# Performance work log

Hardware: AMD Instinct MI355X
Metric: run time of the kernel (lower is better)

Reference implementation:

```python
import jax, jax.numpy as jnp
import numpy as np

B = 1024          # graphs (games)
NPG = 12          # nodes per hand (to_dense_batch max_num_nodes=12)
N = B * NPG       # nodes per node type
EPG = 72          # edges per graph per edge type
E = B * EPG
CARD = 32         # card embedding dim
HID = 256         # hidden_dim
H = 4             # attention heads
L = 3             # num_layers
FIN = 128         # final_dim
LRELU_SLOPE = float(FIN)  # faithful to nn.LeakyReLU(final_dim) bug


def _make_edges(key):
    k1, k2 = jax.random.split(key)
    g = jnp.repeat(jnp.arange(B, dtype=jnp.int32), EPG)
    src = g * NPG + jax.random.randint(k1, (E,), 0, NPG, dtype=jnp.int32)
    dst = g * NPG + jax.random.randint(k2, (E,), 0, NPG, dtype=jnp.int32)
    return jnp.stack([src, dst])


def setup_inputs() -> dict:
    key = jax.random.key(0)
    ks = jax.random.split(key, 24)
    def nrm(k, shape, fan):
        return jax.random.normal(k, shape, jnp.float32) / np.float32(np.sqrt(fan))
    inp = {
        'x_my': jax.random.normal(ks[0], (N, CARD), jnp.float32),
        'x_opp': jax.random.normal(ks[1], (N, CARD), jnp.float32),
        'edge_beats': _make_edges(ks[2]),
        'edge_loses': _make_edges(ks[3]),
        'edge_rev_beats': _make_edges(ks[4]),
        'edge_rev_loses': _make_edges(ks[5]),
        'batch_my': jnp.repeat(jnp.arange(B, dtype=jnp.int32), NPG),
        # input encoder
        'enc_W': nrm(ks[6], (CARD, HID), CARD), 'enc_b': jnp.zeros((HID,), jnp.float32),
        # GATv2 params, axis1 indexes {0: beats(my->opp), 1: rev_loses_to(opp->my)}
        'gat_Wl': nrm(ks[7], (L, 2, HID, H * HID), HID),
        'gat_bl': jnp.zeros((L, 2, H * HID), jnp.float32),
        'gat_Wr': nrm(ks[8], (L, 2, HID, H * HID), HID),
        'gat_br': jnp.zeros((L, 2, H * HID), jnp.float32),
        'gat_att': nrm(ks[9], (L, 2, H, HID), HID),
        'gat_bias': jnp.zeros((L, 2, HID), jnp.float32),
        # CGConv params, axis1 indexes {0: loses_to(my->opp), 1: rev_beats(opp->my)}
        'cg_Wf': nrm(ks[10], (L, 2, 2 * HID, HID), 2 * HID),
        'cg_bf': jnp.zeros((L, 2, HID), jnp.float32),
        'cg_Ws': nrm(ks[11], (L, 2, 2 * HID, HID), 2 * HID),
        'cg_bs': jnp.zeros((L, 2, HID), jnp.float32),
        # nodewise linear per layer
        'node_W': nrm(ks[12], (L, HID, HID), HID),
        'node_b': jnp.zeros((L, HID), jnp.float32),
        # final encoder
        'fin_W1': nrm(ks[13], (HID, FIN), HID), 'fin_b1': jnp.zeros((FIN,), jnp.float32),
        'fin_W2': nrm(ks[14], (FIN, 1), FIN), 'fin_b2': jnp.zeros((1,), jnp.float32),
    }
    return inp


def _gatv2(x_src, x_dst, edge, Wl, bl, Wr, br, att, bias):
    # PyG GATv2Conv, concat=False, add_self_loops=False, negative_slope=0.2
    Nd = x_dst.shape[0]
    xl = (x_src @ Wl + bl).reshape(-1, H, HID)   # [Ns,H,C]
    xr = (x_dst @ Wr + br).reshape(-1, H, HID)   # [Nd,H,C]
    src, dst = edge[0], edge[1]
    e = jax.nn.leaky_relu(xl[src] + xr[dst], 0.2)            # [E,H,C]
    alpha = jnp.einsum('ehc,hc->eh', e, att)                 # [E,H]
    m = jax.ops.segment_max(alpha, dst, num_segments=Nd)     # softmax by dst
    a = jnp.exp(alpha - m[dst])
    denom = jax.ops.segment_sum(a, dst, num_segments=Nd)
    a = a / (denom[dst] + 1e-16)
    out = jax.ops.segment_sum(a[:, :, None] * xl[src], dst, num_segments=Nd)
    return out.mean(axis=1) + bias                           # mean over heads


def _cgconv(x_src, x_dst, edge, Wf, bf, Ws, bs):
    # PyG CGConv: z = [x_i(dst), x_j(src)]; sigmoid gate * softplus; sum; residual
    src, dst = edge[0], edge[1]
    z = jnp.concatenate([x_dst[dst], x_src[src]], axis=-1)   # [E,2*HID]
    msg = jax.nn.sigmoid(z @ Wf + bf) * jax.nn.softplus(z @ Ws + bs)
    return x_dst + jax.ops.segment_sum(msg, dst, num_segments=x_dst.shape[0])


def reference(x_my, x_opp, edge_beats, edge_loses, edge_rev_beats, edge_rev_loses,
              batch_my, enc_W, enc_b, gat_Wl, gat_bl, gat_Wr, gat_br, gat_att,
              gat_bias, cg_Wf, cg_bf, cg_Ws, cg_bs, node_W, node_b,
              fin_W1, fin_b1, fin_W2, fin_b2):
    h_my = x_my @ enc_W + enc_b
    h_opp = x_opp @ enc_W + enc_b
    for l in range(L):
        # destination opponent_hand: GAT(beats) + CG(loses_to)  (HeteroConv aggr='sum')
        opp_new = _gatv2(h_my, h_opp, edge_beats, gat_Wl[l, 0], gat_bl[l, 0],
                         gat_Wr[l, 0], gat_br[l, 0], gat_att[l, 0], gat_bias[l, 0]) \
                + _cgconv(h_my, h_opp, edge_loses, cg_Wf[l, 0], cg_bf[l, 0],
                          cg_Ws[l, 0], cg_bs[l, 0])
        # destination my_hand: CG(rev_beats) + GAT(rev_loses_to)
        my_new = _cgconv(h_opp, h_my, edge_rev_beats, cg_Wf[l, 1], cg_bf[l, 1],
                         cg_Ws[l, 1], cg_bs[l, 1]) \
               + _gatv2(h_opp, h_my, edge_rev_loses, gat_Wl[l, 1], gat_bl[l, 1],
                        gat_Wr[l, 1], gat_br[l, 1], gat_att[l, 1], gat_bias[l, 1])
        h_my = my_new @ node_W[l] + node_b[l]
        h_opp = opp_new @ node_W[l] + node_b[l]
    f = jax.nn.leaky_relu(h_my @ fin_W1 + fin_b1, LRELU_SLOPE)
    logits = f @ fin_W2 + fin_b2                              # [N,1]
    # to_dense_batch with exactly NPG sorted nodes per graph == reshape
    return logits.reshape(B, NPG)
```

## Files before the change

kernel.cpp:

```cpp
#include <hip/hip_runtime.h>

#define NNODES 12288
#define ETOT   73728
#define NGR    1024
#define LOG2E  1.442695041f
#define LN2    0.6931471806f

typedef __attribute__((ext_vector_type(8))) short short8;
typedef __attribute__((ext_vector_type(4))) float f32x4;

__device__ __forceinline__ unsigned short f2b(float f) {
  return __builtin_bit_cast(unsigned short, (__bf16)f);
}
__device__ __forceinline__ float b2f(unsigned short u) {
  return __uint_as_float(((unsigned)u) << 16);
}
__device__ __forceinline__ void load_lds16(const void* g, void* l) {
  __builtin_amdgcn_global_load_lds(
      (const __attribute__((address_space(1))) unsigned int*)g,
      (__attribute__((address_space(3))) unsigned int*)l, 16, 0, 0);
}
__device__ __forceinline__ unsigned fenc(float f) {
  unsigned u = __float_as_uint(f);
  return (u & 0x80000000u) ? ~u : (u | 0x80000000u);
}
__device__ __forceinline__ float fdec(unsigned e) {
  unsigned u = (e & 0x80000000u) ? (e & 0x7FFFFFFFu) : ~e;
  return __uint_as_float(u);
}

__device__ __forceinline__ const unsigned short* pnode(
    const unsigned short* P, int col0, int node) {
  return P + ((size_t)(col0 >> 7) * NNODES + node) * 128 + (col0 & 127);
}

__global__ void pack_kernel(
    const float* __restrict__ gat_Wl, const float* __restrict__ gat_Wr,
    const float* __restrict__ cg_Wf, const float* __restrict__ cg_Ws,
    const float* __restrict__ node_W, const float* __restrict__ enc_W,
    const float* __restrict__ fin_W1,
    const float* __restrict__ gat_bl, const float* __restrict__ gat_br,
    const float* __restrict__ cg_bf, const float* __restrict__ cg_bs,
    const float* __restrict__ x_my, const float* __restrict__ x_opp,
    unsigned short* __restrict__ wt_my, unsigned short* __restrict__ wt_opp,
    unsigned short* __restrict__ node_wt, unsigned short* __restrict__ enc_wt,
    unsigned short* __restrict__ fin_w1t,
    float* __restrict__ bias_my, float* __restrict__ bias_opp,
    unsigned short* __restrict__ xb)
{
  int idx = blockIdx.x * 256 + threadIdx.x;
  if (idx < 2 * 2359296) {
    int which = idx >= 2359296;
    int t = which ? idx - 2359296 : idx;
    int l = t / 786432;
    int r = t - l * 786432;
    int j = r & 7, lane = (r >> 3) & 63, blk = r >> 9;
    int kb = blk & 7, nb = blk >> 3;
    int n = nb * 16 + (lane & 15);
    int k = kb * 32 + (lane >> 4) * 8 + j;
    float v;
    if (!which) {
      if (n < 1024)      v = gat_Wl[((l*2+0)*256 + k)*1024 + n];
      else if (n < 2048) v = gat_Wr[((l*2+1)*256 + k)*1024 + (n-1024)];
      else if (n < 2304) v = cg_Wf[((l*2+0)*512 + 256 + k)*256 + (n-2048)];
      else if (n < 2560) v = cg_Ws[((l*2+0)*512 + 256 + k)*256 + (n-2304)];
      else if (n < 2816) v = cg_Wf[((l*2+1)*512 + k)*256 + (n-2560)];
      else               v = cg_Ws[((l*2+1)*512 + k)*256 + (n-2816)];
      wt_my[t] = f2b(v);
    } else {
      if (n < 1024)      v = gat_Wr[((l*2+0)*256 + k)*1024 + n];
      else if (n < 2048) v = gat_Wl[((l*2+1)*256 + k)*1024 + (n-1024)];
      else if (n < 2304) v = cg_Wf[((l*2+0)*512 + k)*256 + (n-2048)];
      else if (n < 2560) v = cg_Ws[((l*2+0)*512 + k)*256 + (n-2304)];
      else if (n < 2816) v = cg_Wf[((l*2+1)*512 + 256 + k)*256 + (n-2560)];
      else               v = cg_Ws[((l*2+1)*512 + 256 + k)*256 + (n-2816)];
      wt_opp[t] = f2b(v);
    }
    return;
  }
  idx -= 2 * 2359296;
  if (idx < 196608) {
    int l = idx / 65536, r = idx - l * 65536;
    int j = r & 7, lane = (r >> 3) & 63, blk = r >> 9;
    int kb = blk & 7, nb = blk >> 3;
    int n = nb * 16 + (lane & 15);
    int k = kb * 32 + (lane >> 4) * 8 + j;
    node_wt[idx] = f2b(node_W[(l*256 + k)*256 + n]);
    return;
  }
  idx -= 196608;
  if (idx < 8192) {
    int r = idx;
    int j = r & 7, lane = (r >> 3) & 63, blk = r >> 9;
    int nb = blk;
    int n = nb * 16 + (lane & 15);
    int k = (lane >> 4) * 8 + j;
    enc_wt[idx] = f2b(enc_W[k*256 + n]);
    return;
  }
  idx -= 8192;
  if (idx < 32768) {
    int r = idx;
    int j = r & 7, lane = (r >> 3) & 63, blk = r >> 9;
    int kb = blk & 7, nb = blk >> 3;
    int n = nb * 16 + (lane & 15);
    int k = kb * 32 + (lane >> 4) * 8 + j;
    fin_w1t[idx] = f2b(fin_W1[k*128 + n]);
    return;
  }
  idx -= 32768;
  if (idx < 9216) {
    int l = idx / 3072, n = idx - l * 3072;
    float v;
    if (n < 1024)      v = gat_bl[(l*2+0)*1024 + n];
    else if (n < 2048) v = gat_br[(l*2+1)*1024 + (n-1024)];
    else if (n < 2560) v = 0.f;
    else if (n < 2816) v = cg_bf[(l*2+1)*256 + (n-2560)];
    else               v = cg_bs[(l*2+1)*256 + (n-2816)];
    bias_my[idx] = v;
    return;
  }
  idx -= 9216;
  if (idx < 9216) {
    int l = idx / 3072, n = idx - l * 3072;
    float v;
    if (n < 1024)      v = gat_br[(l*2+0)*1024 + n];
    else if (n < 2048) v = gat_bl[(l*2+1)*1024 + (n-1024)];
    else if (n < 2304) v = cg_bf[(l*2+0)*256 + (n-2048)];
    else if (n < 2560) v = cg_bs[(l*2+0)*256 + (n-2304)];
    else               v = 0.f;
    bias_opp[idx] = v;
    return;
  }
  idx -= 9216;
  if (idx < 2 * 393216) {
    xb[idx] = f2b(idx < 393216 ? x_my[idx] : x_opp[idx - 393216]);
  }
}

__global__ __launch_bounds__(256) void gemm64(
    const unsigned short* __restrict__ A, const unsigned short* __restrict__ Ab,
    int lda,
    const unsigned short* __restrict__ Wp, const unsigned short* __restrict__ Wpb,
    const float* __restrict__ bias, const float* __restrict__ biasb,
    unsigned short* __restrict__ C, unsigned short* __restrict__ Cb,
    int ldc, int K, int act, int bx_split)
{
  __shared__ __align__(16) unsigned short lA[64 * 256];
  const int tid = threadIdx.x;
  const int lane = tid & 63;
  const int w = tid >> 6;
  const int wr = w >> 1, wc = w & 1;
  const int r0 = lane & 15, kq = lane >> 4;
  const int KT = K >> 5;
  const int gm = (K >> 3) - 1;
  const int rmask = gm > 7 ? 7 : gm;
  const int gsh = __popc((unsigned)gm);

  const unsigned short *Ap, *Wsel;
  const float* bp;
  unsigned short* Cp;
  int tileM;
  if ((int)blockIdx.x < bx_split) {
    Ap = A;  Wsel = Wp;  bp = bias;  Cp = C;  tileM = blockIdx.x * 64;
  } else {
    Ap = Ab; Wsel = Wpb; bp = biasb; Cp = Cb; tileM = (blockIdx.x - bx_split) * 64;
  }
  const int tileN = blockIdx.y * 128;

  for (int rd = 0; rd < KT; ++rd) {
    int idx = rd * 256 + tid;
    int row = idx >> gsh;
    int g = idx & gm;
    load_lds16(Ap + (size_t)(tileM + row) * lda + ((g ^ (row & rmask)) << 3),
               (char*)lA + idx * 16);
  }

  const int nblk0 = (tileN >> 4) + wc * 4;
  const unsigned short* wn0 = Wsel + ((size_t)(nblk0 + 0) * KT * 64 + lane) * 8;
  const unsigned short* wn1 = Wsel + ((size_t)(nblk0 + 1) * KT * 64 + lane) * 8;
  const unsigned short* wn2 = Wsel + ((size_t)(nblk0 + 2) * KT * 64 + lane) * 8;
  const unsigned short* wn3 = Wsel + ((size_t)(nblk0 + 3) * KT * 64 + lane) * 8;

  short8 b0_0 = *(const short8*)wn0;
  short8 b0_1 = *(const short8*)wn1;
  short8 b0_2 = *(const short8*)wn2;
  short8 b0_3 = *(const short8*)wn3;
  short8 b1_0 = b0_0, b1_1 = b0_1, b1_2 = b0_2, b1_3 = b0_3;
  if (KT > 1) {
    b1_0 = *(const short8*)(wn0 + 512);
    b1_1 = *(const short8*)(wn1 + 512);
    b1_2 = *(const short8*)(wn2 + 512);
    b1_3 = *(const short8*)(wn3 + 512);
  }

  f32x4 acc[2][4];
#pragma unroll
  for (int m = 0; m < 2; ++m)
#pragma unroll
    for (int n = 0; n < 4; ++n)
      acc[m][n] = (f32x4){0.f, 0.f, 0.f, 0.f};

  const int rb0 = (wr * 32 + r0) * K;
  const int rb1 = (wr * 32 + 16 + r0) * K;
  const int rx = r0 & rmask;

  __syncthreads();

  for (int kt = 0; kt < KT; ++kt) {
    short8 b2_0 = b1_0, b2_1 = b1_1, b2_2 = b1_2, b2_3 = b1_3;
    if (kt + 2 < KT) {
      const int o = (kt + 2) * 512;
      b2_0 = *(const short8*)(wn0 + o);
      b2_1 = *(const short8*)(wn1 + o);
      b2_2 = *(const short8*)(wn2 + o);
      b2_3 = *(const short8*)(wn3 + o);
    }
    const int p = (((kt << 2) + kq) ^ rx) * 8;
    short8 af0 = *(const short8*)&lA[rb0 + p];
    short8 af1 = *(const short8*)&lA[rb1 + p];
    acc[0][0] = __builtin_amdgcn_mfma_f32_16x16x32_bf16(b0_0, af0, acc[0][0], 0, 0, 0);
    acc[0][1] = __builtin_amdgcn_mfma_f32_16x16x32_bf16(b0_1, af0, acc[0][1], 0, 0, 0);
    acc[0][2] = __builtin_amdgcn_mfma_f32_16x16x32_bf16(b0_2, af0, acc[0][2], 0, 0, 0);
    acc[0][3] = __builtin_amdgcn_mfma_f32_16x16x32_bf16(b0_3, af0, acc[0][3], 0, 0, 0);
    acc[1][0] = __builtin_amdgcn_mfma_f32_16x16x32_bf16(b0_0, af1, acc[1][0], 0, 0, 0);
    acc[1][1] = __builtin_amdgcn_mfma_f32_16x16x32_bf16(b0_1, af1, acc[1][1], 0, 0, 0);
    acc[1][2] = __builtin_amdgcn_mfma_f32_16x16x32_bf16(b0_2, af1, acc[1][2], 0, 0, 0);
    acc[1][3] = __builtin_amdgcn_mfma_f32_16x16x32_bf16(b0_3, af1, acc[1][3], 0, 0, 0);
    b0_0 = b1_0; b0_1 = b1_1; b0_2 = b1_2; b0_3 = b1_3;
    b1_0 = b2_0; b1_1 = b2_1; b1_2 = b2_2; b1_3 = b2_3;
  }

  unsigned short* cT = lA;
  __syncthreads();
#pragma unroll
  for (int m = 0; m < 2; ++m) {
    const int rl = wr * 32 + m * 16 + r0;
#pragma unroll
    for (int n = 0; n < 4; ++n) {
      const int cl = wc * 64 + n * 16 + kq * 4;
      const f32x4 bv = *(const f32x4*)&bp[tileN + cl];
      float v0 = acc[m][n][0] + bv[0];
      float v1 = acc[m][n][1] + bv[1];
      float v2 = acc[m][n][2] + bv[2];
      float v3 = acc[m][n][3] + bv[3];
      if (act) {
        v0 = v0 > 0.f ? v0 : 128.f * v0;
        v1 = v1 > 0.f ? v1 : 128.f * v1;
        v2 = v2 > 0.f ? v2 : 128.f * v2;
        v3 = v3 > 0.f ? v3 : 128.f * v3;
      }
      uint2 pk;
      pk.x = (unsigned)f2b(v0) | ((unsigned)f2b(v1) << 16);
      pk.y = (unsigned)f2b(v2) | ((unsigned)f2b(v3) << 16);
      *(uint2*)&cT[rl * 132 + cl] = pk;
    }
  }
  __syncthreads();
#pragma unroll
  for (int it = 0; it < 4; ++it) {
    const int idx = it * 256 + tid;
    const int row = idx >> 4, ch = idx & 15;
    const uint4 val = *(const uint4*)&cT[row * 132 + ch * 8];
    *(uint4*)(Cp + (size_t)(tileM + row) * ldc + tileN + ch * 8) = val;
  }
}

__global__ __launch_bounds__(256) void gemm64p(
    const unsigned short* __restrict__ A, const unsigned short* __restrict__ Ab,
    const unsigned short* __restrict__ Wp, const unsigned short* __restrict__ Wpb,
    const float* __restrict__ bias, const float* __restrict__ biasb,
    unsigned short* __restrict__ C, unsigned short* __restrict__ Cb,
    int bx_split)
{
  const int K = 256, KT = 8;
  __shared__ __align__(16) unsigned short lA[64 * 256];
  __shared__ __align__(16) unsigned short cT[64 * 132];
  const int tid = threadIdx.x;
  const int lane = tid & 63;
  const int w = tid >> 6;
  const int wr = w >> 1, wc = w & 1;
  const int r0 = lane & 15, kq = lane >> 4;

  const unsigned short *Ap, *Wsel;
  const float* bp;
  unsigned short* Cp;
  int tileM;
  if ((int)blockIdx.x < bx_split) {
    Ap = A;  Wsel = Wp;  bp = bias;  Cp = C;  tileM = blockIdx.x * 64;
  } else {
    Ap = Ab; Wsel = Wpb; bp = biasb; Cp = Cb; tileM = (blockIdx.x - bx_split) * 64;
  }

  for (int rd = 0; rd < KT; ++rd) {
    int idx = rd * 256 + tid;
    int row = idx >> 5;
    int g = idx & 31;
    load_lds16(Ap + (size_t)(tileM + row) * K + ((g ^ (row & 7)) << 3),
               (char*)lA + idx * 16);
  }

  const int rb0 = (wr * 32 + r0) * K;
  const int rb1 = (wr * 32 + 16 + r0) * K;
  const int rx = r0 & 7;

  __syncthreads();

  for (int nn = 0; nn < 12; ++nn) {
    const int cb = (int)blockIdx.y * 12 + nn;
    const int tileN = cb * 128;
    const int nblk0 = (tileN >> 4) + wc * 4;
    const unsigned short* wn0 = Wsel + ((size_t)(nblk0 + 0) * KT * 64 + lane) * 8;
    const unsigned short* wn1 = Wsel + ((size_t)(nblk0 + 1) * KT * 64 + lane) * 8;
    const unsigned short* wn2 = Wsel + ((size_t)(nblk0 + 2) * KT * 64 + lane) * 8;
    const unsigned short* wn3 = Wsel + ((size_t)(nblk0 + 3) * KT * 64 + lane) * 8;

    short8 b0_0 = *(const short8*)wn0;
    short8 b0_1 = *(const short8*)wn1;
    short8 b0_2 = *(const short8*)wn2;
    short8 b0_3 = *(const short8*)wn3;
    short8 b1_0 = *(const short8*)(wn0 + 512);
    short8 b1_1 = *(const short8*)(wn1 + 512);
    short8 b1_2 = *(const short8*)(wn2 + 512);
    short8 b1_3 = *(const short8*)(wn3 + 512);

    f32x4 acc[2][4];
#pragma unroll
    for (int m = 0; m < 2; ++m)
#pragma unroll
      for (int n = 0; n < 4; ++n)
        acc[m][n] = (f32x4){0.f, 0.f, 0.f, 0.f};

    for (int kt = 0; kt < KT; ++kt) {
      short8 b2_0 = b1_0, b2_1 = b1_1, b2_2 = b1_2, b2_3 = b1_3;
      if (kt + 2 < KT) {
        const int o = (kt + 2) * 512;
        b2_0 = *(const short8*)(wn0 + o);
        b2_1 = *(const short8*)(wn1 + o);
        b2_2 = *(const short8*)(wn2 + o);
        b2_3 = *(const short8*)(wn3 + o);
      }
      const int p = (((kt << 2) + kq) ^ rx) * 8;
      short8 af0 = *(const short8*)&lA[rb0 + p];
      short8 af1 = *(const short8*)&lA[rb1 + p];
      acc[0][0] = __builtin_amdgcn_mfma_f32_16x16x32_bf16(b0_0, af0, acc[0][0], 0, 0, 0);
      acc[0][1] = __builtin_amdgcn_mfma_f32_16x16x32_bf16(b0_1, af0, acc[0][1], 0, 0, 0);
      acc[0][2] = __builtin_amdgcn_mfma_f32_16x16x32_bf16(b0_2, af0, acc[0][2], 0, 0, 0);
      acc[0][3] = __builtin_amdgcn_mfma_f32_16x16x32_bf16(b0_3, af0, acc[0][3], 0, 0, 0);
      acc[1][0] = __builtin_amdgcn_mfma_f32_16x16x32_bf16(b0_0, af1, acc[1][0], 0, 0, 0);
      acc[1][1] = __builtin_amdgcn_mfma_f32_16x16x32_bf16(b0_1, af1, acc[1][1], 0, 0, 0);
      acc[1][2] = __builtin_amdgcn_mfma_f32_16x16x32_bf16(b0_2, af1, acc[1][2], 0, 0, 0);
      acc[1][3] = __builtin_amdgcn_mfma_f32_16x16x32_bf16(b0_3, af1, acc[1][3], 0, 0, 0);
      b0_0 = b1_0; b0_1 = b1_1; b0_2 = b1_2; b0_3 = b1_3;
      b1_0 = b2_0; b1_1 = b2_1; b1_2 = b2_2; b1_3 = b2_3;
    }

    __syncthreads();
#pragma unroll
    for (int m = 0; m < 2; ++m) {
      const int rl = wr * 32 + m * 16 + r0;
#pragma unroll
      for (int n = 0; n < 4; ++n) {
        const int cl = wc * 64 + n * 16 + kq * 4;
        const f32x4 bv = *(const f32x4*)&bp[tileN + cl];
        uint2 pk;
        pk.x = (unsigned)f2b(acc[m][n][0] + bv[0]) |
               ((unsigned)f2b(acc[m][n][1] + bv[1]) << 16);
        pk.y = (unsigned)f2b(acc[m][n][2] + bv[2]) |
               ((unsigned)f2b(acc[m][n][3] + bv[3]) << 16);
        *(uint2*)&cT[rl * 132 + cl] = pk;
      }
    }
    __syncthreads();
    unsigned short* dstb = Cp + ((size_t)cb * NNODES + tileM) * 128;
#pragma unroll
    for (int it = 0; it < 4; ++it) {
      const int idx = it * 256 + tid;
      const uint4 val = *(const uint4*)&cT[(idx >> 4) * 132 + (idx & 15) * 8];
      *(uint4*)(dstb + (size_t)idx * 8) = val;
    }
  }
}

#define SX 260
__global__ __launch_bounds__(256) void gat_edge(
    const unsigned short* __restrict__ proj_my,
    const unsigned short* __restrict__ proj_op,
    const int* __restrict__ e_beats, const int* __restrict__ e_rl,
    const float* __restrict__ attL, const float* __restrict__ gbiasL,
    unsigned short* __restrict__ gat_op, unsigned short* __restrict__ gat_my)
{
  __shared__ __align__(16) unsigned short xl[48 * SX];
  __shared__ __align__(16) float attS[4 * SX];
  __shared__ float alphaU[288];
  __shared__ float wU[288];
  __shared__ unsigned mU[48];
  __shared__ float denS[48];
  __shared__ __align__(16) float A2f[12 * 48];
  __shared__ int pmap[144], multI[144], uniqP[144], nuniqS;
  __shared__ unsigned char se8[72], de8[72];
  const int bid = blockIdx.x, tid = threadIdx.x;
  const int dir = bid >= NGR;
  const int g = dir ? bid - NGR : bid;
  const int base = g * 12;

  const unsigned short *Psrc, *Pdst;
  int pcol0;
  const int* edges;
  const float* att;
  const float* gbias;
  unsigned short* outp;
  if (!dir) {
    Psrc = proj_my; Pdst = proj_op; pcol0 = 0;
    edges = e_beats; att = attL; gbias = gbiasL; outp = gat_op;
  } else {
    Psrc = proj_op; Pdst = proj_my; pcol0 = 1024;
    edges = e_rl; att = attL + 1024; gbias = gbiasL + 256; outp = gat_my;
  }

  if (tid < 72) {
    se8[tid] = (unsigned char)(edges[g * 72 + tid] - base);
    de8[tid] = (unsigned char)(edges[ETOT + g * 72 + tid] - base);
  }
  if (tid < 144) { pmap[tid] = -1; multI[tid] = 0; }
  if (tid == 0) nuniqS = 0;
  if (tid < 48) { mU[tid] = 0u; denS[tid] = 0.f; }
  for (int i = tid; i < 576; i += 256) A2f[i] = 0.f;
  for (int i = tid; i < 1024; i += 256)
    attS[(i >> 8) * SX + (i & 255)] = att[i];
  for (int i = tid; i < 3072; i += 256) {
    int s = i >> 8, c4 = (i & 255) * 4;
    int h = c4 >> 8, cc = c4 & 255;
    *(ushort4*)&xl[(h * 12 + s) * SX + cc] =
        *(const ushort4*)pnode(Psrc, pcol0 + c4, base + s);
  }
  __syncthreads();

  if (tid < 72) {
    const int p = (int)de8[tid] * 12 + (int)se8[tid];
    atomicAdd(&multI[p], 1);
    if (atomicCAS(&pmap[p], -1, 0) == -1) {
      const int u = atomicAdd(&nuniqS, 1);
      uniqP[u] = p;
    }
  }
  __syncthreads();
  const int NU4 = nuniqS * 4;

  for (int t = tid; t < NU4; t += 256) {
    const int u = t >> 2, h = t & 3;
    const int p = uniqP[u];
    const int d = p / 12, s = p - d * 12;
    const unsigned short* prA = pnode(Pdst, pcol0 + h * 256, base + d);
    float sum = 0.f;
#pragma unroll
    for (int half = 0; half < 2; ++half) {
      const unsigned short* pr = prA + (size_t)half * (NNODES * 128);
      const unsigned short* pl = &xl[(h * 12 + s) * SX + half * 128];
      const f32x4* pa = (const f32x4*)&attS[h * SX + half * 128];
      for (int q = 0; q < 32; ++q) {
        ushort4 a4 = *(const ushort4*)(pl + q * 4);
        ushort4 b4 = *(const ushort4*)(pr + q * 4);
        f32x4 av = pa[q];
        float v0 = b2f(a4.x) + b2f(b4.x); v0 = fmaxf(v0, 0.2f * v0);
        float v1 = b2f(a4.y) + b2f(b4.y); v1 = fmaxf(v1, 0.2f * v1);
        float v2 = b2f(a4.z) + b2f(b4.z); v2 = fmaxf(v2, 0.2f * v2);
        float v3 = b2f(a4.w) + b2f(b4.w); v3 = fmaxf(v3, 0.2f * v3);
        sum = fmaf(v0, av.x, sum); sum = fmaf(v1, av.y, sum);
        sum = fmaf(v2, av.z, sum); sum = fmaf(v3, av.w, sum);
      }
    }
    sum *= LOG2E;
    alphaU[t] = sum;
    atomicMax(&mU[d * 4 + h], fenc(sum));
  }
  __syncthreads();

  for (int t = tid; t < NU4; t += 256) {
    const int u = t >> 2, h = t & 3;
    const int p = uniqP[u];
    const int d = p / 12;
    const float m = fdec(mU[d * 4 + h]);
    const float wv = __builtin_amdgcn_exp2f(alphaU[t] - m);
    wU[t] = wv;
    atomicAdd(&denS[d * 4 + h], (float)multI[p] * wv);
  }
  __syncthreads();

  for (int t = tid; t < NU4; t += 256) {
    const int u = t >> 2, h = t & 3;
    const int p = uniqP[u];
    const int d = p / 12, s = p - d * 12;
    const float inv = 0.25f * __builtin_amdgcn_rcpf(denS[d * 4 + h] + 1e-16f);
    A2f[d * 48 + h * 12 + s] = (float)multI[p] * wU[t] * inv;
  }
  __syncthreads();

  {
    const int c = tid;
    float xlv[48];
#pragma unroll
    for (int j = 0; j < 48; ++j) xlv[j] = b2f(xl[j * SX + c]);
    const float gb = gbias[c];
#pragma unroll
    for (int d = 0; d < 12; ++d) {
      const f32x4* arow = (const f32x4*)&A2f[d * 48];
      float s = 0.f;
#pragma unroll
      for (int jj = 0; jj < 12; ++jj) {
        f32x4 a4 = arow[jj];
        s = fmaf(a4.x, xlv[jj * 4 + 0], s);
        s = fmaf(a4.y, xlv[jj * 4 + 1], s);
        s = fmaf(a4.z, xlv[jj * 4 + 2], s);
        s = fmaf(a4.w, xlv[jj * 4 + 3], s);
      }
      outp[(size_t)(base + d) * 256 + c] = f2b(s + gb);
    }
  }
}

__global__ __launch_bounds__(256) void cg_fused(
    const unsigned short* __restrict__ proj_my,
    const unsigned short* __restrict__ proj_op,
    unsigned short* __restrict__ Hmy, unsigned short* __restrict__ Hopp,
    const unsigned short* __restrict__ gat_my, const unsigned short* __restrict__ gat_op,
    const int* __restrict__ e_loses, const int* __restrict__ e_rb,
    const unsigned short* __restrict__ node_wtL, const float* __restrict__ node_bL)
{
  __shared__ __align__(8) unsigned short df[3072], dsb[3072];
  __shared__ __align__(8) unsigned short sfb[3072], ssb[3072];
  __shared__ __align__(16) unsigned short At[16 * 264];
  __shared__ unsigned char srcl[12 * 80];
  __shared__ int cnt[12];
  __shared__ int se_[72], de_[72];
  const int bid = blockIdx.x, tid = threadIdx.x;
  const int dir = bid >= NGR;
  const int g = dir ? bid - NGR : bid;
  const int base = g * 12;

  const unsigned short *Pd, *Ps, *gatp;
  unsigned short *Hout;
  int fcol, scol;
  const int* edges;
  if (!dir) {
    Pd = proj_op; Ps = proj_my; fcol = 2048; scol = 2304;
    Hout = Hopp; gatp = gat_op; edges = e_loses;
  } else {
    Pd = proj_my; Ps = proj_op; fcol = 2560; scol = 2816;
    Hout = Hmy; gatp = gat_my; edges = e_rb;
  }

  if (tid < 72) {
    se_[tid] = edges[g * 72 + tid] - base;
    de_[tid] = edges[ETOT + g * 72 + tid] - base;
  }
  for (int i = tid; i < 768; i += 256) {
    int s = i >> 6, c4 = (i & 63) * 4;
    const int node = base + s;
    *(ushort4*)&df[s * 256 + c4]  = *(const ushort4*)pnode(Pd, fcol + c4, node);
    *(ushort4*)&dsb[s * 256 + c4] = *(const ushort4*)pnode(Pd, scol + c4, node);
    *(ushort4*)&sfb[s * 256 + c4] = *(const ushort4*)pnode(Ps, fcol + c4, node);
    *(ushort4*)&ssb[s * 256 + c4] = *(const ushort4*)pnode(Ps, scol + c4, node);
  }
  const int c = tid;
  float hv[12], gv[12];
#pragma unroll
  for (int d = 0; d < 12; ++d) {
    const size_t o = (size_t)(base + d) * 256 + c;
    hv[d] = b2f(Hout[o]);
    gv[d] = b2f(gatp[o]);
  }
  __syncthreads();
  if (tid < 12) {
    int n = 0;
    for (int e = 0; e < 72; ++e)
      if (de_[e] == tid) srcl[tid * 80 + (n++)] = (unsigned char)se_[e];
    cnt[tid] = n;
  }
  __syncthreads();
  for (int d = 0; d < 12; ++d) {
    const float fd = b2f(df[d * 256 + c]);
    const float sd = b2f(dsb[d * 256 + c]);
    const int n = cnt[d];
    float acc = 0.f;
    for (int j = 0; j < n; ++j) {
      const int s = srcl[d * 80 + j];
      const float zf = fd + b2f(sfb[s * 256 + c]);
      const float zs = sd + b2f(ssb[s * 256 + c]);
      const float gate = __builtin_amdgcn_rcpf(1.f + __builtin_amdgcn_exp2f(-LOG2E * zf));
      const float e2 = __builtin_amdgcn_exp2f(-LOG2E * fabsf(zs));
      const float sp = fmaxf(zs, 0.f) + LN2 * __builtin_amdgcn_logf(1.f + e2);
      acc = fmaf(gate, sp, acc);
    }
    At[d * 264 + c] = f2b(hv[d] + gv[d] + acc);
  }
  __syncthreads();
  {
    const int w = tid >> 6, lane = tid & 63;
    const int r0 = lane & 15, kq = lane >> 4;
#pragma unroll
    for (int n = 0; n < 4; ++n) {
      const unsigned short* wb = node_wtL + ((size_t)(w * 4 + n) * 8) * 512 + lane * 8;
      f32x4 a = (f32x4){0.f, 0.f, 0.f, 0.f};
#pragma unroll
      for (int kt = 0; kt < 8; ++kt) {
        short8 wf = *(const short8*)(wb + kt * 512);
        short8 af = *(const short8*)&At[r0 * 264 + kt * 32 + kq * 8];
        a = __builtin_amdgcn_mfma_f32_16x16x32_bf16(wf, af, a, 0, 0, 0);
      }
      if (r0 < 12) {
        const int col0 = w * 64 + n * 16 + kq * 4;
        const f32x4 bv = *(const f32x4*)&node_bL[col0];
        uint2 pk;
        pk.x = (unsigned)f2b(a[0] + bv[0]) | ((unsigned)f2b(a[1] + bv[1]) << 16);
        pk.y = (unsigned)f2b(a[2] + bv[2]) | ((unsigned)f2b(a[3] + bv[3]) << 16);
        *(uint2*)(Hout + (size_t)(base + r0) * 256 + col0) = pk;
      }
    }
  }
}

__global__ __launch_bounds__(256) void logits_kernel(
    const unsigned short* __restrict__ f, const float* __restrict__ W2,
    const float* __restrict__ b2, float* __restrict__ out)
{
  const int node = blockIdx.x * 4 + (threadIdx.x >> 6);
  const int lane = threadIdx.x & 63;
  const size_t o = (size_t)node * 128 + lane * 2;
  float s = b2f(f[o]) * W2[lane * 2] + b2f(f[o + 1]) * W2[lane * 2 + 1];
  for (int d = 32; d > 0; d >>= 1) s += __shfl_down(s, d, 64);
  if (lane == 0) out[node] = s + b2[0];
}

extern "C" void kernel_launch(void* const* d_in, const int* in_sizes, int n_in,
                              void* d_out, int out_size, void* d_ws, size_t ws_size,
                              hipStream_t stream) {
  const float* x_my    = (const float*)d_in[0];
  const float* x_opp   = (const float*)d_in[1];
  const int*   e_beats = (const int*)d_in[2];
  const int*   e_loses = (const int*)d_in[3];
  const int*   e_rb    = (const int*)d_in[4];
  const int*   e_rl    = (const int*)d_in[5];
  const float* enc_W   = (const float*)d_in[7];
  const float* enc_b   = (const float*)d_in[8];
  const float* gat_Wl  = (const float*)d_in[9];
  const float* gat_bl  = (const float*)d_in[10];
  const float* gat_Wr  = (const float*)d_in[11];
  const float* gat_br  = (const float*)d_in[12];
  const float* gat_att = (const float*)d_in[13];
  const float* gat_bsp = (const float*)d_in[14];
  const float* cg_Wf   = (const float*)d_in[15];
  const float* cg_bf   = (const float*)d_in[16];
  const float* cg_Ws   = (const float*)d_in[17];
  const float* cg_bs   = (const float*)d_in[18];
  const float* node_W  = (const float*)d_in[19];
  const float* node_b  = (const float*)d_in[20];
  const float* fin_W1  = (const float*)d_in[21];
  const float* fin_b1  = (const float*)d_in[22];
  const float* fin_W2  = (const float*)d_in[23];
  const float* fin_b2  = (const float*)d_in[24];

  char* wsp = (char*)d_ws;
  size_t off = 0;
  auto alloc = [&](size_t b) { char* p = wsp + off; off += (b + 255) & ~(size_t)255; return p; };
  unsigned short* wt_my   = (unsigned short*)alloc((size_t)2359296 * 2);
  unsigned short* wt_opp  = (unsigned short*)alloc((size_t)2359296 * 2);
  unsigned short* node_wt = (unsigned short*)alloc((size_t)196608 * 2);
  unsigned short* enc_wt  = (unsigned short*)alloc((size_t)8192 * 2);
  unsigned short* fin_w1t = (unsigned short*)alloc((size_t)32768 * 2);
  float*          bias_my = (float*)alloc((size_t)9216 * 4);
  float*          bias_op = (float*)alloc((size_t)9216 * 4);
  unsigned short* xb      = (unsigned short*)alloc((size_t)786432 * 2);
  unsigned short* Hb      = (unsigned short*)alloc((size_t)2 * NNODES * 256 * 2);
  unsigned short* proj_my = (unsigned short*)alloc((size_t)NNODES * 3072 * 2);
  unsigned short* proj_op = (unsigned short*)alloc((size_t)NNODES * 3072 * 2);
  unsigned short* gat_my  = (unsigned short*)alloc((size_t)NNODES * 256 * 2);
  unsigned short* gat_op  = (unsigned short*)alloc((size_t)NNODES * 256 * 2);
  unsigned short* fbuf    = (unsigned short*)alloc((size_t)NNODES * 128 * 2);

  const int PACK_TOTAL = 2 * 2359296 + 196608 + 8192 + 32768 + 2 * 9216 + 2 * 393216;
  pack_kernel<<<(PACK_TOTAL + 255) / 256, 256, 0, stream>>>(
      gat_Wl, gat_Wr, cg_Wf, cg_Ws, node_W, enc_W, fin_W1,
      gat_bl, gat_br, cg_bf, cg_bs, x_my, x_opp,
      wt_my, wt_opp, node_wt, enc_wt, fin_w1t, bias_my, bias_op, xb);

  unsigned short* Hmy  = Hb;
  unsigned short* Hopp = Hb + (size_t)NNODES * 256;

  gemm64<<<dim3(384, 2), 256, 0, stream>>>(
      xb, xb, 32, enc_wt, enc_wt, enc_b, enc_b, Hb, Hb, 256, 32, 0, 384);

  for (int l = 0; l < 3; ++l) {
    gemm64p<<<dim3(384, 2), 256, 0, stream>>>(
        Hmy, Hopp,
        wt_my + (size_t)l * 786432, wt_opp + (size_t)l * 786432,
        bias_my + l * 3072, bias_op + l * 3072,
        proj_my, proj_op, 192);
    gat_edge<<<2 * NGR, 256, 0, stream>>>(
        proj_my, proj_op, e_beats, e_rl,
        gat_att + l * 2048, gat_bsp + l * 512, gat_op, gat_my);
    cg_fused<<<2 * NGR, 256, 0, stream>>>(
        proj_my, proj_op, Hmy, Hopp, gat_my, gat_op,
        e_loses, e_rb,
        node_wt + (size_t)l * 65536, node_b + l * 256);
  }

  gemm64<<<dim3(192, 1), 256, 0, stream>>>(
      Hmy, Hmy, 256, fin_w1t, fin_w1t, fin_b1, fin_b1, fbuf, fbuf, 128, 256, 1, 192);
  logits_kernel<<<NNODES / 4, 256, 0, stream>>>(fbuf, fin_W2, fin_b2, (float*)d_out);
}
```

Baseline: 516.2 us.

## Compute GAT attention scores with 16-lane groups per destination-head and shuffle softmax

Replaces the per-unique-edge serial 256-channel dot products and shared-memory atomic max/sum passes with a layout where each 16-lane group owns one (destination, head) pair. Each lane handles 16 channels, reduces with cross-lane shuffles, and then does the softmax max and denominator in registers. This removes several barriers, the float-encoded atomics and the long serial loop per thread, and spreads the global reads of destination projections across lanes. The cost is redundant work for destinations with few sources. The code also assumes at most 16 distinct sources per destination, which holds because a hand has 12 nodes.

```diff
diff --git a/kernel.cpp b/kernel.cpp
--- a/kernel.cpp
+++ b/kernel.cpp
@@ -19,14 +19,6 @@
   __builtin_amdgcn_global_load_lds(
       (const __attribute__((address_space(1))) unsigned int*)g,
       (__attribute__((address_space(3))) unsigned int*)l, 16, 0, 0);
-}
-__device__ __forceinline__ unsigned fenc(float f) {
-  unsigned u = __float_as_uint(f);
-  return (u & 0x80000000u) ? ~u : (u | 0x80000000u);
-}
-__device__ __forceinline__ float fdec(unsigned e) {
-  unsigned u = (e & 0x80000000u) ? (e & 0x7FFFFFFFu) : ~e;
-  return __uint_as_float(u);
 }
 
 __device__ __forceinline__ const unsigned short* pnode(
@@ -392,13 +384,11 @@
 {
   __shared__ __align__(16) unsigned short xl[48 * SX];
   __shared__ __align__(16) float attS[4 * SX];
-  __shared__ float alphaU[288];
-  __shared__ float wU[288];
-  __shared__ unsigned mU[48];
-  __shared__ float denS[48];
   __shared__ __align__(16) float A2f[12 * 48];
-  __shared__ int pmap[144], multI[144], uniqP[144], nuniqS;
-  __shared__ unsigned char se8[72], de8[72];
+  __shared__ int multI[144];
+  __shared__ unsigned char srcG[12][12];
+  __shared__ unsigned char multG[12][12];
+  __shared__ int cntG[12];
   const int bid = blockIdx.x, tid = threadIdx.x;
   const int dir = bid >= NGR;
   const int g = dir ? bid - NGR : bid;
@@ -418,14 +408,14 @@
     edges = e_rl; att = attL + 1024; gbias = gbiasL + 256; outp = gat_my;
   }
 
+  if (tid < 144) multI[tid] = 0;
+  for (int i = tid; i < 576; i += 256) A2f[i] = 0.f;
+  __syncthreads();
   if (tid < 72) {
-    se8[tid] = (unsigned char)(edges[g * 72 + tid] - base);
-    de8[tid] = (unsigned char)(edges[ETOT + g * 72 + tid] - base);
-  }
-  if (tid < 144) { pmap[tid] = -1; multI[tid] = 0; }
-  if (tid == 0) nuniqS = 0;
-  if (tid < 48) { mU[tid] = 0u; denS[tid] = 0.f; }
-  for (int i = tid; i < 576; i += 256) A2f[i] = 0.f;
+    const int s = edges[g * 72 + tid] - base;
+    const int d = edges[ETOT + g * 72 + tid] - base;
+    atomicAdd(&multI[d * 12 + s], 1);
+  }
   for (int i = tid; i < 1024; i += 256)
     attS[(i >> 8) * SX + (i & 255)] = att[i];
   for (int i = tid; i < 3072; i += 256) {
@@ -436,63 +426,88 @@
   }
   __syncthreads();
 
-  if (tid < 72) {
-    const int p = (int)de8[tid] * 12 + (int)se8[tid];
-    atomicAdd(&multI[p], 1);
-    if (atomicCAS(&pmap[p], -1, 0) == -1) {
-      const int u = atomicAdd(&nuniqS, 1);
-      uniqP[u] = p;
-    }
-  }
-  __syncthreads();
-  const int NU4 = nuniqS * 4;
-
-  for (int t = tid; t < NU4; t += 256) {
-    const int u = t >> 2, h = t & 3;
-    const int p = uniqP[u];
-    const int d = p / 12, s = p - d * 12;
-    const unsigned short* prA = pnode(Pdst, pcol0 + h * 256, base + d);
-    float sum = 0.f;
-#pragma unroll
-    for (int half = 0; half < 2; ++half) {
-      const unsigned short* pr = prA + (size_t)half * (NNODES * 128);
-      const unsigned short* pl = &xl[(h * 12 + s) * SX + half * 128];
-      const f32x4* pa = (const f32x4*)&attS[h * SX + half * 128];
-      for (int q = 0; q < 32; ++q) {
-        ushort4 a4 = *(const ushort4*)(pl + q * 4);
-        ushort4 b4 = *(const ushort4*)(pr + q * 4);
-        f32x4 av = pa[q];
-        float v0 = b2f(a4.x) + b2f(b4.x); v0 = fmaxf(v0, 0.2f * v0);
-        float v1 = b2f(a4.y) + b2f(b4.y); v1 = fmaxf(v1, 0.2f * v1);
-        float v2 = b2f(a4.z) + b2f(b4.z); v2 = fmaxf(v2, 0.2f * v2);
-        float v3 = b2f(a4.w) + b2f(b4.w); v3 = fmaxf(v3, 0.2f * v3);
-        sum = fmaf(v0, av.x, sum); sum = fmaf(v1, av.y, sum);
-        sum = fmaf(v2, av.z, sum); sum = fmaf(v3, av.w, sum);
-      }
-    }
-    sum *= LOG2E;
-    alphaU[t] = sum;
-    atomicMax(&mU[d * 4 + h], fenc(sum));
-  }
-  __syncthreads();
-
-  for (int t = tid; t < NU4; t += 256) {
-    const int u = t >> 2, h = t & 3;
-    const int p = uniqP[u];
-    const int d = p / 12;
-    const float m = fdec(mU[d * 4 + h]);
-    const float wv = __builtin_amdgcn_exp2f(alphaU[t] - m);
-    wU[t] = wv;
-    atomicAdd(&denS[d * 4 + h], (float)multI[p] * wv);
-  }
-  __syncthreads();
-
-  for (int t = tid; t < NU4; t += 256) {
-    const int u = t >> 2, h = t & 3;
-    const int p = uniqP[u];
-    const int d = p / 12, s = p - d * 12;
-    const float inv = 0.25f * __builtin_amdgcn_rcpf(denS[d * 4 + h] + 1e-16f);
-    A2f[d * 48 + h * 12 + s] = (float)multI[p] * wU[t] * inv;
+  if (tid < 12) {
+    int n = 0;
+    for (int s = 0; s < 12; ++s) {
+      const int m = multI[tid * 12 + s];
+      if (m > 0) { srcG[tid][n] = (unsigned char)s; multG[tid][n] = (unsigned char)m; ++n; }
+    }
+    cntG[tid] = n;
+  }
+  __syncthreads();
+
+  for (int r = 0; r < 3; ++r) {
+    const int slot = r * 256 + tid;
+    const int g16 = slot >> 4, lane16 = slot & 15;
+    const int d = g16 >> 2, h = g16 & 3;
+    const int cnt = cntG[d];
+    const int ch0 = lane16 * 16;
+    const unsigned short* prp = pnode(Pdst, pcol0 + h * 256 + ch0, base + d);
+    const ushort4 xr0 = *(const ushort4*)(prp);
+    const ushort4 xr1 = *(const ushort4*)(prp + 4);
+    const ushort4 xr2 = *(const ushort4*)(prp + 8);
+    const ushort4 xr3 = *(const ushort4*)(prp + 12);
+    const float* pa = &attS[h * SX + ch0];
+    const f32x4 at0 = *(const f32x4*)(pa);
+    const f32x4 at1 = *(const f32x4*)(pa + 4);
+    const f32x4 at2 = *(const f32x4*)(pa + 8);
+    const f32x4 at3 = *(const f32x4*)(pa + 12);
+
+    float myalpha = -1e30f;
+    for (int j = 0; j < cnt; ++j) {
+      const int s = srcG[d][j];
+      const unsigned short* pl = &xl[(h * 12 + s) * SX + ch0];
+      float p = 0.f;
+      {
+        ushort4 a4 = *(const ushort4*)(pl);
+        float v0 = b2f(a4.x) + b2f(xr0.x); v0 = fmaxf(v0, 0.2f * v0);
+        float v1 = b2f(a4.y) + b2f(xr0.y); v1 = fmaxf(v1, 0.2f * v1);
+        float v2 = b2f(a4.z) + b2f(xr0.z); v2 = fmaxf(v2, 0.2f * v2);
+        float v3 = b2f(a4.w) + b2f(xr0.w); v3 = fmaxf(v3, 0.2f * v3);
+        p = fmaf(v0, at0[0], p); p = fmaf(v1, at0[1], p);
+        p = fmaf(v2, at0[2], p); p = fmaf(v3, at0[3], p);
+      }
+      {
+        ushort4 a4 = *(const ushort4*)(pl + 4);
+        float v0 = b2f(a4.x) + b2f(xr1.x); v0 = fmaxf(v0, 0.2f * v0);
+        float v1 = b2f(a4.y) + b2f(xr1.y); v1 = fmaxf(v1, 0.2f * v1);
+        float v2 = b2f(a4.z) + b2f(xr1.z); v2 = fmaxf(v2, 0.2f * v2);
+        float v3 = b2f(a4.w) + b2f(xr1.w); v3 = fmaxf(v3, 0.2f * v3);
+        p = fmaf(v0, at1[0], p); p = fmaf(v1, at1[1], p);
+        p = fmaf(v2, at1[2], p); p = fmaf(v3, at1[3], p);
+      }
+      {
+        ushort4 a4 = *(const ushort4*)(pl + 8);
+        float v0 = b2f(a4.x) + b2f(xr2.x); v0 = fmaxf(v0, 0.2f * v0);
+        float v1 = b2f(a4.y) + b2f(xr2.y); v1 = fmaxf(v1, 0.2f * v1);
+        float v2 = b2f(a4.z) + b2f(xr2.z); v2 = fmaxf(v2, 0.2f * v2);
+        float v3 = b2f(a4.w) + b2f(xr2.w); v3 = fmaxf(v3, 0.2f * v3);
+        p = fmaf(v0, at2[0], p); p = fmaf(v1, at2[1], p);
+        p = fmaf(v2, at2[2], p); p = fmaf(v3, at2[3], p);
+      }
+      {
+        ushort4 a4 = *(const ushort4*)(pl + 12);
+        float v0 = b2f(a4.x) + b2f(xr3.x); v0 = fmaxf(v0, 0.2f * v0);
+        float v1 = b2f(a4.y) + b2f(xr3.y); v1 = fmaxf(v1, 0.2f * v1);
+        float v2 = b2f(a4.z) + b2f(xr3.z); v2 = fmaxf(v2, 0.2f * v2);
+        float v3 = b2f(a4.w) + b2f(xr3.w); v3 = fmaxf(v3, 0.2f * v3);
+        p = fmaf(v0, at3[0], p); p = fmaf(v1, at3[1], p);
+        p = fmaf(v2, at3[2], p); p = fmaf(v3, at3[3], p);
+      }
+#pragma unroll
+      for (int off = 1; off < 16; off <<= 1) p += __shfl_xor(p, off, 64);
+      if (j == lane16) myalpha = p * LOG2E;
+    }
+    float m = myalpha;
+#pragma unroll
+    for (int off = 1; off < 16; off <<= 1) m = fmaxf(m, __shfl_xor(m, off, 64));
+    const float wv = __builtin_amdgcn_exp2f(myalpha - m);
+    const float mw = (lane16 < cnt) ? (float)multG[d][lane16] * wv : 0.f;
+    float den = mw;
+#pragma unroll
+    for (int off = 1; off < 16; off <<= 1) den += __shfl_xor(den, off, 64);
+    const float inv = 0.25f * __builtin_amdgcn_rcpf(den + 1e-16f);
+    if (lane16 < cnt) A2f[d * 48 + h * 12 + srcG[d][lane16]] = mw * inv;
   }
   __syncthreads();
 
```

Measured after the change: 494.1 us. 1.04x faster.
